# Performance work log

Hardware: AMD Instinct MI355X
Metric: run time of the kernel (lower is better)

The kernel has to match this reference:

```python
import jax, jax.numpy as jnp
import numpy as np

B, S, H = 8, 4096, 1152
LENGTH = 256


def setup_inputs() -> dict:
    key = jax.random.key(0)
    k1, k2 = jax.random.split(key)
    hidden_states = jax.random.normal(k1, (B, S, H), dtype=jnp.float32)
    # (x, y) patch coordinates on a 64x64 grid
    patch_positions = jax.random.randint(k2, (B, S, 2), 0, 64, dtype=jnp.int64)
    padding_positions = jnp.ones((B, LENGTH), dtype=jnp.bool_)
    return {
        "hidden_states": hidden_states,
        "patch_positions": patch_positions,
        "padding_positions": padding_positions,
    }


def _pool(hidden_states, patch_positions, length):
    b, s, h = hidden_states.shape
    k = int((s // length) ** 0.5)
    k_sq = k * k
    assert k_sq * length == s
    clamped = jnp.maximum(patch_positions, 0)  # clamp(min=0)
    max_x = jnp.max(clamped[..., 0], axis=-1, keepdims=True) + 1  # [B,1]
    kidx = clamped // k
    kernel_idxs = kidx[..., 0] + (max_x // k) * kidx[..., 1]  # [B,S], values < length
    # segment-mean instead of the one-hot GEMM: identical math
    seg = (kernel_idxs + length * jnp.arange(b, dtype=kernel_idxs.dtype)[:, None]).reshape(-1)
    pooled = jax.ops.segment_sum(
        hidden_states.reshape(b * s, h), seg, num_segments=b * length
    ).reshape(b, length, h) / k_sq
    counts = jax.ops.segment_sum(
        jnp.ones((b * s,), dtype=jnp.int32), seg, num_segments=b * length
    ).reshape(b, length)
    mask = counts > 0  # equivalent to ~(weights == 0).all(dim=1)
    return pooled, mask


def reference(hidden_states, patch_positions, padding_positions):
    length = LENGTH
    if hidden_states.shape[1] == length:
        pooled, mask = hidden_states, padding_positions
    else:
        pooled, mask = _pool(hidden_states, patch_positions, length)
    root_hidden_size = float(hidden_states.shape[-1]) ** 0.5
    pooled = pooled * root_hidden_size
    return pooled, mask
```

## Files before the change

### kernel.cpp

```cpp
#include <hip/hip_runtime.h>
#include <hip/hip_bf16.h>

#define NB 8
#define NS 4096
#define NH 1152
#define LEN 256
#define F4ROW (NH / 4)

typedef float vf4 __attribute__((ext_vector_type(4)));

__global__ __launch_bounds__(256) void gvp_fused(
        const float* __restrict__ hidden,
        const int* __restrict__ patch,
        float* __restrict__ out,
        float* __restrict__ maskout) {
    int g = blockIdx.x;
    int b = g >> 8;
    int myseg = g & (LEN - 1);
    int t = threadIdx.x;

    __shared__ __align__(16) int rows[NS];
    __shared__ int s_max[4];
    __shared__ int s_cnt;
    __shared__ int s_mult;
    if (t == 0) s_cnt = 0;

    const int2* p2 = (const int2*)(patch + (size_t)b * NS * 2);
    int pk[16];
    int m = 0;
    #pragma unroll
    for (int i = 0; i < 16; ++i) {
        int2 v = p2[t + 256 * i];
        int x = v.x < 0 ? 0 : v.x;
        int y = v.y < 0 ? 0 : v.y;
        pk[i] = x | (y << 16);
        m = max(m, x);
    }
    #pragma unroll
    for (int off = 32; off > 0; off >>= 1)
        m = max(m, __shfl_down(m, off, 64));
    if ((t & 63) == 0) s_max[t >> 6] = m;
    __syncthreads();
    if (t == 0)
        s_mult = (max(max(s_max[0], s_max[1]), max(s_max[2], s_max[3])) + 1) >> 2;
    __syncthreads();
    int mult = s_mult;

    #pragma unroll
    for (int i = 0; i < 16; ++i) {
        int x = pk[i] & 0xffff;
        int y = pk[i] >> 16;
        int seg = (x >> 2) + mult * (y >> 2);
        if (seg == myseg) {
            int pos = atomicAdd(&s_cnt, 1);
            rows[pos] = t + 256 * i;
        }
    }
    __syncthreads();
    int cnt = s_cnt;

    const float* hb = hidden + (size_t)b * NS * NH;
    vf4 a0 = 0.f, a1 = 0.f;
    int r = 0;
    for (; r + 7 < cnt; r += 8) {
        const vf4* p0 = (const vf4*)(hb + (size_t)rows[r + 0] * NH);
        const vf4* p1 = (const vf4*)(hb + (size_t)rows[r + 1] * NH);
        const vf4* p2r = (const vf4*)(hb + (size_t)rows[r + 2] * NH);
        const vf4* p3 = (const vf4*)(hb + (size_t)rows[r + 3] * NH);
        const vf4* p4 = (const vf4*)(hb + (size_t)rows[r + 4] * NH);
        const vf4* p5 = (const vf4*)(hb + (size_t)rows[r + 5] * NH);
        const vf4* p6 = (const vf4*)(hb + (size_t)rows[r + 6] * NH);
        const vf4* p7 = (const vf4*)(hb + (size_t)rows[r + 7] * NH);
        vf4 v0 = p0[t], v1 = p1[t], v2 = p2r[t], v3 = p3[t];
        vf4 v4 = p4[t], v5 = p5[t], v6 = p6[t], v7 = p7[t];
        v0 += v1; v2 += v3; v4 += v5; v6 += v7;
        v0 += v2; v4 += v6;
        a0 += v0; a1 += v4;
    }
    for (; r < cnt; ++r) {
        const vf4* p0 = (const vf4*)(hb + (size_t)rows[r] * NH);
        a0 += p0[t];
    }
    a0 += a1;

    int l = t & 31;
    int grp = t >> 5;
    vf4 a2 = 0.f;
    for (int r2 = grp; r2 < cnt; r2 += 8) {
        const vf4* p = (const vf4*)(hb + (size_t)rows[r2] * NH);
        a2 += p[256 + l];
    }
    __syncthreads();
    vf4* red = (vf4*)rows;
    red[t] = a2;
    __syncthreads();

    const float scale = 2.1213203435596424f;
    vf4* og = (vf4*)(out + (size_t)g * NH);
    og[t] = a0 * scale;
    if (t < 32) {
        vf4 s = 0.f;
        #pragma unroll
        for (int j = 0; j < 8; ++j) s += red[j * 32 + t];
        og[256 + t] = s * scale;
    }
    if (t == 0) maskout[g] = (cnt > 0) ? 1.0f : 0.0f;
}

extern "C" void kernel_launch(void* const* d_in, const int* in_sizes, int n_in,
                              void* d_out, int out_size, void* d_ws, size_t ws_size,
                              hipStream_t stream) {
    const float* hidden = (const float*)d_in[0];
    const int*   patch  = (const int*)d_in[1];
    float* out = (float*)d_out;
    float* maskout = out + (size_t)NB * LEN * NH;

    gvp_fused<<<NB * LEN, 256, 0, stream>>>(hidden, patch, out, maskout);
}
```

Baseline: 31.94 us.

## Use persistent work-stealing blocks per batch with bounded shared row list

Launches 128 blocks per batch instead of one block per segment. Each block loads and reduces the batch's patch positions once, then takes segments dynamically from a per-batch atomic counter. This amortizes the patch scan and max reduction over several segments and balances uneven segment sizes. Shared row storage shrinks to 256 entries, with a windowed fallback for larger segments. It also adds a memset launch and a serialized atomic queue.

```diff
diff --git a/kernel.cpp b/kernel.cpp
--- a/kernel.cpp
+++ b/kernel.cpp
@@ -5,25 +5,27 @@
 #define NS 4096
 #define NH 1152
 #define LEN 256
-#define F4ROW (NH / 4)
+#define WPB 128
+#define CAP 256
 
 typedef float vf4 __attribute__((ext_vector_type(4)));
 
 __global__ __launch_bounds__(256) void gvp_fused(
         const float* __restrict__ hidden,
         const int* __restrict__ patch,
+        int* __restrict__ qcnt,
         float* __restrict__ out,
         float* __restrict__ maskout) {
-    int g = blockIdx.x;
-    int b = g >> 8;
-    int myseg = g & (LEN - 1);
+    int w = blockIdx.x;
+    int b = w / WPB;
     int t = threadIdx.x;
+    int l = t & 31;
+    int grp = t >> 5;
 
-    __shared__ __align__(16) int rows[NS];
+    __shared__ int rows[CAP];
+    __shared__ vf4 s_red[256];
     __shared__ int s_max[4];
-    __shared__ int s_cnt;
-    __shared__ int s_mult;
-    if (t == 0) s_cnt = 0;
+    __shared__ int s_cnt, s_q, s_mult;
 
     const int2* p2 = (const int2*)(patch + (size_t)b * NS * 2);
     int pk[16];
@@ -46,65 +48,85 @@
     __syncthreads();
     int mult = s_mult;
 
-    #pragma unroll
-    for (int i = 0; i < 16; ++i) {
-        int x = pk[i] & 0xffff;
-        int y = pk[i] >> 16;
-        int seg = (x >> 2) + mult * (y >> 2);
-        if (seg == myseg) {
-            int pos = atomicAdd(&s_cnt, 1);
-            rows[pos] = t + 256 * i;
+    const float scale = 2.1213203435596424f;
+    const float* hb = hidden + (size_t)b * NS * NH;
+
+    int q = w & (WPB - 1);
+    while (q < LEN) {
+        vf4 a0 = 0.f, a1 = 0.f, a2 = 0.f;
+
+        auto gather = [&](int n) {
+            int r = 0;
+            for (; r + 7 < n; r += 8) {
+                const vf4* p0 = (const vf4*)(hb + (size_t)rows[r + 0] * NH);
+                const vf4* p1 = (const vf4*)(hb + (size_t)rows[r + 1] * NH);
+                const vf4* p2r = (const vf4*)(hb + (size_t)rows[r + 2] * NH);
+                const vf4* p3 = (const vf4*)(hb + (size_t)rows[r + 3] * NH);
+                const vf4* p4 = (const vf4*)(hb + (size_t)rows[r + 4] * NH);
+                const vf4* p5 = (const vf4*)(hb + (size_t)rows[r + 5] * NH);
+                const vf4* p6 = (const vf4*)(hb + (size_t)rows[r + 6] * NH);
+                const vf4* p7 = (const vf4*)(hb + (size_t)rows[r + 7] * NH);
+                vf4 v0 = p0[t], v1 = p1[t], v2 = p2r[t], v3 = p3[t];
+                vf4 v4 = p4[t], v5 = p5[t], v6 = p6[t], v7 = p7[t];
+                v0 += v1; v2 += v3; v4 += v5; v6 += v7;
+                v0 += v2; v4 += v6;
+                a0 += v0; a1 += v4;
+            }
+            for (; r < n; ++r)
+                a0 += ((const vf4*)(hb + (size_t)rows[r] * NH))[t];
+            for (int r2 = grp; r2 < n; r2 += 8)
+                a2 += ((const vf4*)(hb + (size_t)rows[r2] * NH))[256 + l];
+        };
+
+        if (t == 0) s_cnt = 0;
+        __syncthreads();
+        #pragma unroll
+        for (int i = 0; i < 16; ++i) {
+            int x = pk[i] & 0xffff, y = pk[i] >> 16;
+            int seg = (x >> 2) + mult * (y >> 2);
+            if (seg == q) {
+                int pos = atomicAdd(&s_cnt, 1);
+                if (pos < CAP) rows[pos] = t + 256 * i;
+            }
         }
+        __syncthreads();
+        int cnt = s_cnt;
+
+        if (cnt <= CAP) {
+            gather(cnt);
+        } else {
+            for (int win = 0; win < 16; ++win) {
+                __syncthreads();
+                if (t == 0) s_cnt = 0;
+                __syncthreads();
+                int x = pk[win] & 0xffff, y = pk[win] >> 16;
+                int seg = (x >> 2) + mult * (y >> 2);
+                if (seg == q) rows[atomicAdd(&s_cnt, 1)] = t + 256 * win;
+                __syncthreads();
+                gather(s_cnt);
+            }
+        }
+
+        a0 += a1;
+        s_red[t] = a2;
+        __syncthreads();
+
+        int g = (b << 8) + q;
+        vf4* og = (vf4*)(out + (size_t)g * NH);
+        og[t] = a0 * scale;
+        if (t < 32) {
+            vf4 s = 0.f;
+            #pragma unroll
+            for (int j = 0; j < 8; ++j) s += s_red[j * 32 + t];
+            og[256 + t] = s * scale;
+        }
+        if (t == 0) {
+            maskout[g] = (cnt > 0) ? 1.0f : 0.0f;
+            s_q = WPB + atomicAdd(&qcnt[b], 1);
+        }
+        __syncthreads();
+        q = s_q;
     }
-    __syncthreads();
-    int cnt = s_cnt;
-
-    const float* hb = hidden + (size_t)b * NS * NH;
-    vf4 a0 = 0.f, a1 = 0.f;
-    int r = 0;
-    for (; r + 7 < cnt; r += 8) {
-        const vf4* p0 = (const vf4*)(hb + (size_t)rows[r + 0] * NH);
-        const vf4* p1 = (const vf4*)(hb + (size_t)rows[r + 1] * NH);
-        const vf4* p2r = (const vf4*)(hb + (size_t)rows[r + 2] * NH);
-        const vf4* p3 = (const vf4*)(hb + (size_t)rows[r + 3] * NH);
-        const vf4* p4 = (const vf4*)(hb + (size_t)rows[r + 4] * NH);
-        const vf4* p5 = (const vf4*)(hb + (size_t)rows[r + 5] * NH);
-        const vf4* p6 = (const vf4*)(hb + (size_t)rows[r + 6] * NH);
-        const vf4* p7 = (const vf4*)(hb + (size_t)rows[r + 7] * NH);
-        vf4 v0 = p0[t], v1 = p1[t], v2 = p2r[t], v3 = p3[t];
-        vf4 v4 = p4[t], v5 = p5[t], v6 = p6[t], v7 = p7[t];
-        v0 += v1; v2 += v3; v4 += v5; v6 += v7;
-        v0 += v2; v4 += v6;
-        a0 += v0; a1 += v4;
-    }
-    for (; r < cnt; ++r) {
-        const vf4* p0 = (const vf4*)(hb + (size_t)rows[r] * NH);
-        a0 += p0[t];
-    }
-    a0 += a1;
-
-    int l = t & 31;
-    int grp = t >> 5;
-    vf4 a2 = 0.f;
-    for (int r2 = grp; r2 < cnt; r2 += 8) {
-        const vf4* p = (const vf4*)(hb + (size_t)rows[r2] * NH);
-        a2 += p[256 + l];
-    }
-    __syncthreads();
-    vf4* red = (vf4*)rows;
-    red[t] = a2;
-    __syncthreads();
-
-    const float scale = 2.1213203435596424f;
-    vf4* og = (vf4*)(out + (size_t)g * NH);
-    og[t] = a0 * scale;
-    if (t < 32) {
-        vf4 s = 0.f;
-        #pragma unroll
-        for (int j = 0; j < 8; ++j) s += red[j * 32 + t];
-        og[256 + t] = s * scale;
-    }
-    if (t == 0) maskout[g] = (cnt > 0) ? 1.0f : 0.0f;
 }
 
 extern "C" void kernel_launch(void* const* d_in, const int* in_sizes, int n_in,
@@ -114,6 +136,8 @@
     const int*   patch  = (const int*)d_in[1];
     float* out = (float*)d_out;
     float* maskout = out + (size_t)NB * LEN * NH;
+    int* qcnt = (int*)d_ws;
 
-    gvp_fused<<<NB * LEN, 256, 0, stream>>>(hidden, patch, out, maskout);
+    hipMemsetAsync(qcnt, 0, NB * sizeof(int), stream);
+    gvp_fused<<<NB * WPB, 256, 0, stream>>>(hidden, patch, qcnt, out, maskout);
 }
```

Result: slower. 47.76 us (+49.5%).

## Split into prep kernel building per-segment row lists and a gather kernel

Applied to the files above, without the earlier changes.

Previously each of the 2048 blocks re-read all 4096 patch positions for its batch and scanned them to find its own segment's rows. A separate 8-block prep kernel now computes segment ids, counts, prefix-sum starts and a bucketed row order once per batch into workspace. The gather blocks then read only their own row list. Padding the row list to a multiple of eight removes the tail loop, and the padded contributions are subtracted afterwards. The cost is an extra kernel launch plus a serialized, low-parallelism prep stage.

```diff
diff --git a/kernel.cpp b/kernel.cpp
--- a/kernel.cpp
+++ b/kernel.cpp
@@ -5,41 +5,41 @@
 #define NS 4096
 #define NH 1152
 #define LEN 256
-#define F4ROW (NH / 4)
 
 typedef float vf4 __attribute__((ext_vector_type(4)));
 
-__global__ __launch_bounds__(256) void gvp_fused(
-        const float* __restrict__ hidden,
-        const int* __restrict__ patch,
-        float* __restrict__ out,
+#define WS_COUNTS 0
+#define WS_STARTS 2048
+#define WS_ORDER  4096
+
+__global__ __launch_bounds__(256) void gvp_prep(
+        const int* __restrict__ patch, int* __restrict__ ws,
         float* __restrict__ maskout) {
-    int g = blockIdx.x;
-    int b = g >> 8;
-    int myseg = g & (LEN - 1);
+    int b = blockIdx.x;
     int t = threadIdx.x;
-
-    __shared__ __align__(16) int rows[NS];
+    __shared__ int s_seg[NS];
+    __shared__ int s_cnt[LEN];
+    __shared__ int s_cur[LEN];
+    __shared__ int sd[LEN];
     __shared__ int s_max[4];
-    __shared__ int s_cnt;
     __shared__ int s_mult;
-    if (t == 0) s_cnt = 0;
 
     const int2* p2 = (const int2*)(patch + (size_t)b * NS * 2);
-    int pk[16];
+    int xs[16], ys[16];
     int m = 0;
     #pragma unroll
     for (int i = 0; i < 16; ++i) {
         int2 v = p2[t + 256 * i];
         int x = v.x < 0 ? 0 : v.x;
         int y = v.y < 0 ? 0 : v.y;
-        pk[i] = x | (y << 16);
+        xs[i] = x; ys[i] = y;
         m = max(m, x);
     }
     #pragma unroll
     for (int off = 32; off > 0; off >>= 1)
         m = max(m, __shfl_down(m, off, 64));
     if ((t & 63) == 0) s_max[t >> 6] = m;
+    s_cnt[t] = 0;
     __syncthreads();
     if (t == 0)
         s_mult = (max(max(s_max[0], s_max[1]), max(s_max[2], s_max[3])) + 1) >> 2;
@@ -48,21 +48,63 @@
 
     #pragma unroll
     for (int i = 0; i < 16; ++i) {
-        int x = pk[i] & 0xffff;
-        int y = pk[i] >> 16;
-        int seg = (x >> 2) + mult * (y >> 2);
-        if (seg == myseg) {
-            int pos = atomicAdd(&s_cnt, 1);
-            rows[pos] = t + 256 * i;
-        }
+        int seg = (xs[i] >> 2) + mult * (ys[i] >> 2);
+        s_seg[t + 256 * i] = seg;
+        atomicAdd(&s_cnt[seg], 1);
     }
     __syncthreads();
-    int cnt = s_cnt;
+
+    int c = s_cnt[t];
+    sd[t] = c;
+    __syncthreads();
+    for (int off = 1; off < 256; off <<= 1) {
+        int v = (t >= off) ? sd[t - off] : 0;
+        __syncthreads();
+        sd[t] += v;
+        __syncthreads();
+    }
+    int base = sd[t] - c;
+    s_cur[t] = base;
+    ws[WS_STARTS + b * LEN + t] = b * NS + base;
+    ws[WS_COUNTS + b * LEN + t] = c;
+    maskout[b * LEN + t] = (c > 0) ? 1.0f : 0.0f;
+    __syncthreads();
+
+    #pragma unroll
+    for (int i = 0; i < 16; ++i) {
+        int s = t + 256 * i;
+        int pos = atomicAdd(&s_cur[s_seg[s]], 1);
+        ws[WS_ORDER + b * NS + pos] = s;
+    }
+}
+
+__global__ __launch_bounds__(256) void gvp_gather(
+        const float* __restrict__ hidden,
+        const int* __restrict__ ws,
+        float* __restrict__ out) {
+    __shared__ __align__(16) int rows[NS + 8];
+    int g = blockIdx.x;
+    int b = g >> 8;
+    int t = threadIdx.x;
+    int start = ws[WS_STARTS + g];
+    int cnt   = ws[WS_COUNTS + g];
+    for (int i = t; i < cnt; i += 256) rows[i] = ws[WS_ORDER + start + i];
+    __syncthreads();
+
+    vf4* og = (vf4*)(out + (size_t)g * NH);
+    if (cnt == 0) {
+        og[t] = 0.f;
+        if (t < 32) og[256 + t] = 0.f;
+        return;
+    }
+    int cnt8 = (cnt + 7) & ~7;
+    int pad = cnt8 - cnt;
+    if (t < pad) rows[cnt + t] = rows[0];
+    __syncthreads();
 
     const float* hb = hidden + (size_t)b * NS * NH;
     vf4 a0 = 0.f, a1 = 0.f;
-    int r = 0;
-    for (; r + 7 < cnt; r += 8) {
+    for (int r = 0; r < cnt8; r += 8) {
         const vf4* p0 = (const vf4*)(hb + (size_t)rows[r + 0] * NH);
         const vf4* p1 = (const vf4*)(hb + (size_t)rows[r + 1] * NH);
         const vf4* p2r = (const vf4*)(hb + (size_t)rows[r + 2] * NH);
@@ -77,26 +119,24 @@
         v0 += v2; v4 += v6;
         a0 += v0; a1 += v4;
     }
-    for (; r < cnt; ++r) {
-        const vf4* p0 = (const vf4*)(hb + (size_t)rows[r] * NH);
-        a0 += p0[t];
+    a0 += a1;
+    if (pad) {
+        vf4 v = ((const vf4*)(hb + (size_t)rows[0] * NH))[t];
+        float fp = (float)pad;
+        a0.x -= fp * v.x; a0.y -= fp * v.y; a0.z -= fp * v.z; a0.w -= fp * v.w;
     }
-    a0 += a1;
 
     int l = t & 31;
     int grp = t >> 5;
     vf4 a2 = 0.f;
-    for (int r2 = grp; r2 < cnt; r2 += 8) {
-        const vf4* p = (const vf4*)(hb + (size_t)rows[r2] * NH);
-        a2 += p[256 + l];
-    }
+    for (int r2 = grp; r2 < cnt; r2 += 8)
+        a2 += ((const vf4*)(hb + (size_t)rows[r2] * NH))[256 + l];
     __syncthreads();
     vf4* red = (vf4*)rows;
     red[t] = a2;
     __syncthreads();
 
     const float scale = 2.1213203435596424f;
-    vf4* og = (vf4*)(out + (size_t)g * NH);
     og[t] = a0 * scale;
     if (t < 32) {
         vf4 s = 0.f;
@@ -104,7 +144,6 @@
         for (int j = 0; j < 8; ++j) s += red[j * 32 + t];
         og[256 + t] = s * scale;
     }
-    if (t == 0) maskout[g] = (cnt > 0) ? 1.0f : 0.0f;
 }
 
 extern "C" void kernel_launch(void* const* d_in, const int* in_sizes, int n_in,
@@ -114,6 +153,8 @@
     const int*   patch  = (const int*)d_in[1];
     float* out = (float*)d_out;
     float* maskout = out + (size_t)NB * LEN * NH;
+    int* ws = (int*)d_ws;
 
-    gvp_fused<<<NB * LEN, 256, 0, stream>>>(hidden, patch, out, maskout);
+    gvp_prep  <<<NB,       256, 0, stream>>>(patch, ws, maskout);
+    gvp_gather<<<NB * LEN, 256, 0, stream>>>(hidden, ws, out);
 }
```

New measurement: 36.04 us. 1.13x slower.
